# Kernel tuning notes

Measured on AMD Instinct MI355X. Metric: run time of the kernel, lower is better.

Reference implementation:

```python
import jax, jax.numpy as jnp
import numpy as np

B, S, D, H, V, C = 64, 512, 512, 512, 32000, 1000
FF = 1024

def setup_inputs() -> dict:
    key = jax.random.key(0)
    ks = jax.random.split(key, 12)
    s = 0.02
    return {
        "tokens": jax.random.randint(ks[0], (B, S), 0, V),
        "emb": jax.random.normal(ks[1], (V, D), jnp.float32) * s,
        "Wx": jax.random.normal(ks[2], (D, H), jnp.float32) * s,
        "Wh": jax.random.normal(ks[3], (H, H), jnp.float32) * s,
        "b_rnn": jnp.zeros((H,), jnp.float32),
        "W1": jax.random.normal(ks[4], (H, FF), jnp.float32) * s,
        "b1": jnp.zeros((FF,), jnp.float32),
        "W2": jax.random.normal(ks[5], (FF, FF), jnp.float32) * s,
        "b2": jnp.zeros((FF,), jnp.float32),
        "Wo": jax.random.normal(ks[6], (FF, C), jnp.float32) * s,
        "bo": jnp.zeros((C,), jnp.float32),
    }

def reference(tokens, emb, Wx, Wh, b_rnn, W1, b1, W2, b2, Wo, bo):
    # Embedding with mask_zero=True: token 0 is a masked timestep
    x = emb[tokens]                                   # [B,S,D]
    mask = (tokens != 0)                              # [B,S]
    # Precompute input projection for all timesteps (hoisted out of the scan)
    xproj = jnp.einsum('bsd,dh->bsh', x, Wx) + b_rnn  # [B,S,H]

    def step(h, inp):
        xp, m = inp                                   # [B,H], [B]
        h_new = jax.nn.relu(xp + h @ Wh)
        # Keras masking: masked steps carry previous state forward
        h = jnp.where(m[:, None], h_new, h)
        return h, None

    h0 = jnp.zeros((B, H), xproj.dtype)
    h, _ = jax.lax.scan(step, h0, (xproj.transpose(1, 0, 2), mask.T))

    y = jax.nn.relu(h @ W1 + b1)
    y = jax.nn.relu(y @ W2 + b2)
    return jax.nn.softmax(y @ Wo + bo, axis=-1)       # [B,C]
```

## Files before the change

kernel.cpp:

```cpp
#include <hip/hip_runtime.h>
#include <stdint.h>

typedef _Float16 half2_t __attribute__((ext_vector_type(2)));
typedef short bf16x8 __attribute__((ext_vector_type(8)));
typedef float f32x4 __attribute__((ext_vector_type(4)));
typedef int i32x4 __attribute__((ext_vector_type(4)));
typedef int i32x8 __attribute__((ext_vector_type(8)));
typedef unsigned short u16;
typedef unsigned int u32;
typedef unsigned long long u64;

#define B_ 64
#define S_ 512
#define D_ 512
#define H_ 512
#define FF_ 1024
#define C_ 1000

#define SW4 128.0f
#define SH4 256.0f

__device__ __forceinline__ u16 f2bf(float f){
  u32 u = __builtin_bit_cast(u32, f);
  u = (u + 0x7FFFu + ((u >> 16) & 1u)) >> 16;
  return (u16)u;
}
__device__ __forceinline__ u32 pkbf(float a, float b){
  return (u32)f2bf(a) | ((u32)f2bf(b) << 16);
}
__device__ __forceinline__ u32 packh2(float a, float b){
  u16 lo = __builtin_bit_cast(u16, (_Float16)a);
  u16 hi = __builtin_bit_cast(u16, (_Float16)b);
  return (u32)lo | ((u32)hi << 16);
}
__device__ __forceinline__ float fdot2u(u32 a, u32 b, float c){
  return __builtin_amdgcn_fdot2(__builtin_bit_cast(half2_t, a),
                                __builtin_bit_cast(half2_t, b), c, false);
}
__device__ __forceinline__ float h2f(u16 h){
  return (float)__builtin_bit_cast(_Float16, h);
}
__device__ __forceinline__ float fp4val(u32 c){
  int e = (c >> 1) & 3;
  float m = 1.0f + 0.5f * (float)(c & 1);
  return (e == 0) ? 0.5f * (float)(c & 1) : m * (float)(1 << (e - 1));
}

__global__ void k_trans_cvt(const float* __restrict__ src, u16* __restrict__ dst){
  __shared__ u16 t[64][65];
  int bx = blockIdx.x & 7, by = blockIdx.x >> 3;
  int tid = threadIdx.x;
  int c = tid & 63, r0 = (tid >> 6) * 16;
  #pragma unroll
  for (int i = 0; i < 16; i++){
    int k = by * 64 + r0 + i, n = bx * 64 + c;
    t[r0 + i][c] = f2bf(src[k * 512 + n]);
  }
  __syncthreads();
  #pragma unroll
  for (int i = 0; i < 16; i++){
    int n = bx * 64 + r0 + i, k = by * 64 + c;
    dst[n * 512 + k] = t[c][r0 + i];
  }
}

__global__ void k_prep_w4(const float* __restrict__ Wh, uint4* __restrict__ Wf4){
  int g = blockIdx.x * 256 + threadIdx.x;
  int fidx = g >> 6, l = g & 63;
  int wv = fidx >> 4, ct = (fidx >> 2) & 3, kt = fidx & 3;
  int q = l >> 4, n = wv * 64 + ct * 16 + (l & 15);
  int k0 = kt * 128 + q * 32;
  u32 d[4] = {0u, 0u, 0u, 0u};
  #pragma unroll
  for (int j = 0; j < 32; j++){
    float w = Wh[(size_t)(k0 + j) * 512 + n] * SW4;
    float aw = fabsf(w);
    u32 s = (w < 0.f) ? 8u : 0u;
    u32 c;
    if (aw < 2.f) c = (u32)(int)rintf(aw * 2.f);
    else if (aw < 4.f) c = 4u + (u32)(int)rintf(aw - 2.f);
    else { c = 6u + (u32)(int)rintf((aw - 4.f) * 0.5f); if (c > 7u) c = 7u; }
    d[j >> 3] |= (c | s) << (4 * (j & 7));
  }
  uint4 o; o.x = d[0]; o.y = d[1]; o.z = d[2]; o.w = d[3];
  Wf4[(size_t)fidx * 64 + l] = o;
}

__global__ void k_mask(const int* __restrict__ tokens, unsigned char* __restrict__ masks8){
  int i = blockIdx.x * 256 + threadIdx.x;
  masks8[i] = (tokens[i] != 0) ? 1 : 0;
}

__global__ void k_pack_pairs(const float* __restrict__ src, u32* __restrict__ dst, int N){
  int n = blockIdx.x * 256 + threadIdx.x;
  int p = blockIdx.y;
  if (n >= N) return;
  dst[p * N + n] = packh2(src[(2 * p) * N + n], src[(2 * p + 1) * N + n]);
}

__global__ __launch_bounds__(256) void k_gemm(const int* __restrict__ tokens,
                                              const float* __restrict__ emb,
                                              const u16* __restrict__ Bt,
                                              const float* __restrict__ bias,
                                              u16* __restrict__ out){
  __shared__ __align__(16) u16 As[128 * 40];
  __shared__ __align__(16) u16 Bs[128 * 40];
  int tid = threadIdx.x;
  int m0 = blockIdx.x * 128, n0 = blockIdx.y * 128;
  int w = tid >> 6, l = tid & 63;
  int wr = w >> 1, wc = w & 1;
  int kg = l >> 4, r16 = l & 15;
  f32x4 acc[4][4];
  #pragma unroll
  for (int mi = 0; mi < 4; mi++)
    #pragma unroll
    for (int ni = 0; ni < 4; ni++) acc[mi][ni] = (f32x4){0.f, 0.f, 0.f, 0.f};
  int srow = tid >> 1, spart = tid & 1;
  int tk = tokens[m0 + srow];
  for (int kt = 0; kt < 512; kt += 32){
    const float4* se = (const float4*)(emb + (size_t)tk * 512 + kt + spart * 16);
    float4 f0 = se[0], f1 = se[1], f2 = se[2], f3 = se[3];
    uint4 a0, a1;
    a0.x = pkbf(f0.x, f0.y); a0.y = pkbf(f0.z, f0.w);
    a0.z = pkbf(f1.x, f1.y); a0.w = pkbf(f1.z, f1.w);
    a1.x = pkbf(f2.x, f2.y); a1.y = pkbf(f2.z, f2.w);
    a1.z = pkbf(f3.x, f3.y); a1.w = pkbf(f3.z, f3.w);
    const uint4* sb = (const uint4*)(Bt + (size_t)(n0 + srow) * 512 + kt);
    uint4 b0 = sb[spart * 2], b1 = sb[spart * 2 + 1];
    uint4* da = (uint4*)(As + srow * 40 + spart * 16);
    da[0] = a0; da[1] = a1;
    uint4* db = (uint4*)(Bs + srow * 40 + spart * 16);
    db[0] = b0; db[1] = b1;
    __syncthreads();
    bf16x8 af[4], bfr[4];
    #pragma unroll
    for (int mi = 0; mi < 4; mi++)
      af[mi] = *(const bf16x8*)(As + (wr * 64 + mi * 16 + r16) * 40 + kg * 8);
    #pragma unroll
    for (int ni = 0; ni < 4; ni++)
      bfr[ni] = *(const bf16x8*)(Bs + (wc * 64 + ni * 16 + r16) * 40 + kg * 8);
    #pragma unroll
    for (int mi = 0; mi < 4; mi++)
      #pragma unroll
      for (int ni = 0; ni < 4; ni++)
        acc[mi][ni] = __builtin_amdgcn_mfma_f32_16x16x32_bf16(af[mi], bfr[ni], acc[mi][ni], 0, 0, 0);
    __syncthreads();
  }
  #pragma unroll
  for (int ni = 0; ni < 4; ni++){
    int col = n0 + wc * 64 + ni * 16 + r16;
    float bb = bias[col];
    #pragma unroll
    for (int mi = 0; mi < 4; mi++){
      int mb = m0 + wr * 64 + mi * 16 + kg * 4;
      #pragma unroll
      for (int r = 0; r < 4; r++){
        float v = (acc[mi][ni][r] + bb) * SH4;
        out[(size_t)(mb + r) * 512 + col] = __builtin_bit_cast(u16, (_Float16)v);
      }
    }
  }
}

__global__ __launch_bounds__(512, 2) void k_rnn(
    const uint4* __restrict__ Wf4, const u16* __restrict__ xproj,
    const unsigned char* __restrict__ masks8, u32* __restrict__ hpack){
  __shared__ __align__(16) unsigned char g4[2][256];
  __shared__ unsigned char msk[512];
  int b = blockIdx.x, tid = threadIdx.x;
  int wv = tid >> 6, l = tid & 63, q = l >> 4, n16 = l & 15;
  int col = wv * 64 + q * 16 + n16;

  i32x8 wgt[16];
  #pragma unroll
  for (int ct = 0; ct < 4; ct++)
    #pragma unroll
    for (int kt = 0; kt < 4; kt++){
      int fidx = (wv * 4 + ct) * 4 + kt;
      uint4 wl = Wf4[(size_t)fidx * 64 + l];
      i32x8 w8 = {(int)wl.x, (int)wl.y, (int)wl.z, (int)wl.w, 0, 0, 0, 0};
      wgt[ct * 4 + kt] = w8;
    }

  msk[tid] = masks8[b * 512 + tid];
  if (tid < 64) ((u32*)g4[0])[tid] = 0;
  __syncthreads();

  const u16* xp = xproj + (size_t)b * S_ * H_;
  u16 xraw = xp[col];
  u32 greg = 0;

  #pragma unroll 1
  for (int t = 0; t < 512; t++){
    u16 xnext = 0;
    if (t < 511) xnext = xp[(size_t)(t + 1) * 512 + col];
    bool wr = msk[t] != 0;
    const unsigned char* gc = g4[t & 1];

    f32x4 acc0 = {0.f,0.f,0.f,0.f}, acc1 = {0.f,0.f,0.f,0.f};
    f32x4 acc2 = {0.f,0.f,0.f,0.f}, acc3 = {0.f,0.f,0.f,0.f};
    #pragma unroll
    for (int kt = 0; kt < 4; kt++){
      i32x4 av = *(const i32x4*)(gc + kt * 64 + q * 16);
      i32x8 a8 = {av[0], av[1], av[2], av[3], 0, 0, 0, 0};
      acc0 = __builtin_amdgcn_mfma_scale_f32_16x16x128_f8f6f4(
          a8, wgt[0 * 4 + kt], acc0, 4, 4, 0, 127, 0, 127);
      acc1 = __builtin_amdgcn_mfma_scale_f32_16x16x128_f8f6f4(
          a8, wgt[1 * 4 + kt], acc1, 4, 4, 0, 127, 0, 127);
      acc2 = __builtin_amdgcn_mfma_scale_f32_16x16x128_f8f6f4(
          a8, wgt[2 * 4 + kt], acc2, 4, 4, 0, 127, 0, 127);
      acc3 = __builtin_amdgcn_mfma_scale_f32_16x16x128_f8f6f4(
          a8, wgt[3 * 4 + kt], acc3, 4, 4, 0, 127, 0, 127);
    }

    float av = (q == 0) ? acc0[0] : (q == 1) ? acc1[0] : (q == 2) ? acc2[0] : acc3[0];
    float gn = fmaxf(fmaf(av, 1.0f / SW4, h2f(xraw)), 0.f);
    u32 code;
    if (gn < 2.f) code = (u32)(int)rintf(gn * 2.f);
    else if (gn < 4.f) code = 4u + (u32)(int)rintf(gn - 2.f);
    else { u32 c = 6u + (u32)(int)rintf((gn - 4.f) * 0.5f); code = c > 7u ? 7u : c; }
    u32 pc = (u32)__shfl_xor((int)code, 1);
    u32 byte = (n16 & 1) ? (pc | (code << 4)) : (code | (pc << 4));
    if (wr) greg = byte;
    if ((l & 1) == 0) g4[(t + 1) & 1][col >> 1] = (unsigned char)greg;
    xraw = xnext;
    __syncthreads();
  }

  if (tid < 256){
    u32 byte = g4[0][tid];
    float f0 = fp4val(byte & 15u) * (1.0f / SH4);
    float f1 = fp4val(byte >> 4) * (1.0f / SH4);
    hpack[b * 256 + tid] = packh2(f0, f1);
  }
}

__global__ __launch_bounds__(256) void k_tail(const u32* __restrict__ hpack,
    const u32* __restrict__ W1p, const float* __restrict__ b1,
    const u32* __restrict__ W2p, const float* __restrict__ b2,
    const u32* __restrict__ Wop, const float* __restrict__ bo,
    float* __restrict__ out){
  __shared__ __align__(16) u32 rowA[512];
  __shared__ __align__(16) u32 rowB[512];
  __shared__ float redm[4], reds[4];
  int b = blockIdx.x, tid = threadIdx.x;
  rowA[tid] = hpack[b * 256 + tid];
  __syncthreads();

  float s0 = 0.f, s1 = 0.f, s2 = 0.f, s3 = 0.f;
  #pragma unroll 2
  for (int p = 0; p < 256; p += 4){
    uint4 h4 = *(const uint4*)&rowA[p];
    const u32* wp = W1p + (size_t)p * FF_ + tid;
    s0 = fdot2u(wp[0], h4.x, s0); s1 = fdot2u(wp[256], h4.x, s1);
    s2 = fdot2u(wp[512], h4.x, s2); s3 = fdot2u(wp[768], h4.x, s3);
    s0 = fdot2u(wp[FF_ + 0], h4.y, s0); s1 = fdot2u(wp[FF_ + 256], h4.y, s1);
    s2 = fdot2u(wp[FF_ + 512], h4.y, s2); s3 = fdot2u(wp[FF_ + 768], h4.y, s3);
    s0 = fdot2u(wp[2*FF_ + 0], h4.z, s0); s1 = fdot2u(wp[2*FF_ + 256], h4.z, s1);
    s2 = fdot2u(wp[2*FF_ + 512], h4.z, s2); s3 = fdot2u(wp[2*FF_ + 768], h4.z, s3);
    s0 = fdot2u(wp[3*FF_ + 0], h4.w, s0); s1 = fdot2u(wp[3*FF_ + 256], h4.w, s1);
    s2 = fdot2u(wp[3*FF_ + 512], h4.w, s2); s3 = fdot2u(wp[3*FF_ + 768], h4.w, s3);
  }
  {
    float y0 = fmaxf(s0 + b1[tid], 0.f);
    float y1 = fmaxf(s1 + b1[tid + 256], 0.f);
    float y2 = fmaxf(s2 + b1[tid + 512], 0.f);
    float y3 = fmaxf(s3 + b1[tid + 768], 0.f);
    float o0 = __shfl_xor(y0, 1), o1 = __shfl_xor(y1, 1);
    float o2 = __shfl_xor(y2, 1), o3 = __shfl_xor(y3, 1);
    if ((tid & 1) == 0){
      int i = tid >> 1;
      rowB[i] = packh2(y0, o0); rowB[128 + i] = packh2(y1, o1);
      rowB[256 + i] = packh2(y2, o2); rowB[384 + i] = packh2(y3, o3);
    }
  }
  __syncthreads();

  s0 = s1 = s2 = s3 = 0.f;
  #pragma unroll 2
  for (int p = 0; p < 512; p += 4){
    uint4 h4 = *(const uint4*)&rowB[p];
    const u32* wp = W2p + (size_t)p * FF_ + tid;
    s0 = fdot2u(wp[0], h4.x, s0); s1 = fdot2u(wp[256], h4.x, s1);
    s2 = fdot2u(wp[512], h4.x, s2); s3 = fdot2u(wp[768], h4.x, s3);
    s0 = fdot2u(wp[FF_ + 0], h4.y, s0); s1 = fdot2u(wp[FF_ + 256], h4.y, s1);
    s2 = fdot2u(wp[FF_ + 512], h4.y, s2); s3 = fdot2u(wp[FF_ + 768], h4.y, s3);
    s0 = fdot2u(wp[2*FF_ + 0], h4.z, s0); s1 = fdot2u(wp[2*FF_ + 256], h4.z, s1);
    s2 = fdot2u(wp[2*FF_ + 512], h4.z, s2); s3 = fdot2u(wp[2*FF_ + 768], h4.z, s3);
    s0 = fdot2u(wp[3*FF_ + 0], h4.w, s0); s1 = fdot2u(wp[3*FF_ + 256], h4.w, s1);
    s2 = fdot2u(wp[3*FF_ + 512], h4.w, s2); s3 = fdot2u(wp[3*FF_ + 768], h4.w, s3);
  }
  {
    float y0 = fmaxf(s0 + b2[tid], 0.f);
    float y1 = fmaxf(s1 + b2[tid + 256], 0.f);
    float y2 = fmaxf(s2 + b2[tid + 512], 0.f);
    float y3 = fmaxf(s3 + b2[tid + 768], 0.f);
    float o0 = __shfl_xor(y0, 1), o1 = __shfl_xor(y1, 1);
    float o2 = __shfl_xor(y2, 1), o3 = __shfl_xor(y3, 1);
    if ((tid & 1) == 0){
      int i = tid >> 1;
      rowA[i] = packh2(y0, o0); rowA[128 + i] = packh2(y1, o1);
      rowA[256 + i] = packh2(y2, o2); rowA[384 + i] = packh2(y3, o3);
    }
  }
  __syncthreads();

  int n0 = tid, n1 = tid + 256, n2 = tid + 512, n3 = tid + 768;
  bool v3 = n3 < C_;
  int n3c = v3 ? n3 : 0;
  float z0 = 0.f, z1 = 0.f, z2 = 0.f, z3 = 0.f;
  #pragma unroll 4
  for (int p = 0; p < 512; p++){
    u32 y = rowA[p];
    z0 = fdot2u(Wop[p * C_ + n0], y, z0);
    z1 = fdot2u(Wop[p * C_ + n1], y, z1);
    z2 = fdot2u(Wop[p * C_ + n2], y, z2);
    z3 = fdot2u(Wop[p * C_ + n3c], y, z3);
  }
  z0 += bo[n0]; z1 += bo[n1]; z2 += bo[n2]; z3 += bo[n3c];
  float mx = fmaxf(fmaxf(z0, z1), z2);
  if (v3) mx = fmaxf(mx, z3);
  #pragma unroll
  for (int o = 1; o < 64; o <<= 1) mx = fmaxf(mx, __shfl_xor(mx, o));
  if ((tid & 63) == 0) redm[tid >> 6] = mx;
  __syncthreads();
  mx = fmaxf(fmaxf(redm[0], redm[1]), fmaxf(redm[2], redm[3]));
  float e0 = __expf(z0 - mx), e1 = __expf(z1 - mx), e2 = __expf(z2 - mx);
  float e3 = v3 ? __expf(z3 - mx) : 0.f;
  float s = e0 + e1 + e2 + e3;
  #pragma unroll
  for (int o = 1; o < 64; o <<= 1) s += __shfl_xor(s, o);
  if ((tid & 63) == 0) reds[tid >> 6] = s;
  __syncthreads();
  s = reds[0] + reds[1] + reds[2] + reds[3];
  float inv = 1.0f / s;
  out[b * C_ + n0] = e0 * inv;
  out[b * C_ + n1] = e1 * inv;
  out[b * C_ + n2] = e2 * inv;
  if (v3) out[b * C_ + n3] = e3 * inv;
}

extern "C" void kernel_launch(void* const* d_in, const int* in_sizes, int n_in,
                              void* d_out, int out_size, void* d_ws, size_t ws_size,
                              hipStream_t stream) {
  const int*   tokens = (const int*)d_in[0];
  const float* emb    = (const float*)d_in[1];
  const float* Wx     = (const float*)d_in[2];
  const float* Wh     = (const float*)d_in[3];
  const float* brnn   = (const float*)d_in[4];
  const float* W1     = (const float*)d_in[5];
  const float* b1     = (const float*)d_in[6];
  const float* W2     = (const float*)d_in[7];
  const float* b2     = (const float*)d_in[8];
  const float* Wo     = (const float*)d_in[9];
  const float* bo     = (const float*)d_in[10];
  float* out = (float*)d_out;

  char* ws = (char*)d_ws;
  size_t off = 0;
  auto alloc = [&](size_t bytes) -> void* {
    void* p = ws + off;
    off += (bytes + 255) & ~(size_t)255;
    return p;
  };
  u16* WxT    = (u16*)alloc((size_t)512 * 512 * 2);
  u16* xproj  = (u16*)alloc((size_t)32768 * 512 * 2);
  uint4* Wf4  = (uint4*)alloc((size_t)128 * 64 * 16);
  unsigned char* masks8 = (unsigned char*)alloc(32768);
  u32* W1p    = (u32*)alloc((size_t)256 * 1024 * 4);
  u32* W2p    = (u32*)alloc((size_t)512 * 1024 * 4);
  u32* Wop    = (u32*)alloc((size_t)512 * 1000 * 4);
  u32* hpack  = (u32*)alloc((size_t)64 * 256 * 4);

  k_trans_cvt<<<dim3(64), dim3(256), 0, stream>>>(Wx, WxT);
  k_prep_w4<<<dim3(32), dim3(256), 0, stream>>>(Wh, Wf4);
  k_mask<<<dim3(128), dim3(256), 0, stream>>>(tokens, masks8);
  k_pack_pairs<<<dim3(4, 256), dim3(256), 0, stream>>>(W1, W1p, 1024);
  k_pack_pairs<<<dim3(4, 512), dim3(256), 0, stream>>>(W2, W2p, 1024);
  k_pack_pairs<<<dim3(4, 512), dim3(256), 0, stream>>>(Wo, Wop, 1000);
  k_gemm<<<dim3(256, 4), dim3(256), 0, stream>>>(tokens, emb, WxT, brnn, xproj);
  k_rnn<<<dim3(64), dim3(512), 0, stream>>>(Wf4, xproj, masks8, hpack);
  k_tail<<<dim3(64), dim3(256), 0, stream>>>(hpack, W1p, b1, W2p, b2, Wop, bo, out);
}
```

Measured before the change: 421.7 us.

## Pre-convert embedding table to bf16 and load GEMM fragments directly from global

Adds a kernel that converts the whole 32000x512 embedding table to bf16 once per call. The input-projection GEMM then reads MFMA fragments straight from global memory, with no shared-memory staging or barriers, and each block covers all 512 output columns for 64 rows. The goal is to drop the per-tile fp32-to-bf16 conversion and the __syncthreads stalls. In exchange it converts the full 65MB table even though only 32768 rows are gathered, and the global fragment loads are less coalesced.

```diff
diff --git a/kernel.cpp b/kernel.cpp
--- a/kernel.cpp
+++ b/kernel.cpp
@@ -16,6 +16,7 @@
 #define H_ 512
 #define FF_ 1024
 #define C_ 1000
+#define V_ 32000
 
 #define SW4 128.0f
 #define SH4 256.0f
@@ -44,6 +45,16 @@
   int e = (c >> 1) & 3;
   float m = 1.0f + 0.5f * (float)(c & 1);
   return (e == 0) ? 0.5f * (float)(c & 1) : m * (float)(1 << (e - 1));
+}
+
+__global__ void k_cvt_emb(const float* __restrict__ src, u16* __restrict__ dst){
+  int c = blockIdx.x * 256 + threadIdx.x;
+  const float4* s = (const float4*)(src + (size_t)c * 8);
+  float4 a = s[0], b = s[1];
+  uint4 o;
+  o.x = pkbf(a.x, a.y); o.y = pkbf(a.z, a.w);
+  o.z = pkbf(b.x, b.y); o.w = pkbf(b.z, b.w);
+  *(uint4*)(dst + (size_t)c * 8) = o;
 }
 
 __global__ void k_trans_cvt(const float* __restrict__ src, u16* __restrict__ dst){
@@ -98,61 +109,51 @@
   dst[p * N + n] = packh2(src[(2 * p) * N + n], src[(2 * p + 1) * N + n]);
 }
 
-__global__ __launch_bounds__(256) void k_gemm(const int* __restrict__ tokens,
-                                              const float* __restrict__ emb,
-                                              const u16* __restrict__ Bt,
+__global__ __launch_bounds__(512) void k_gemm(const int* __restrict__ tokens,
+                                              const u16* __restrict__ embbf,
+                                              const u16* __restrict__ WxT,
                                               const float* __restrict__ bias,
                                               u16* __restrict__ out){
-  __shared__ __align__(16) u16 As[128 * 40];
-  __shared__ __align__(16) u16 Bs[128 * 40];
   int tid = threadIdx.x;
-  int m0 = blockIdx.x * 128, n0 = blockIdx.y * 128;
-  int w = tid >> 6, l = tid & 63;
-  int wr = w >> 1, wc = w & 1;
-  int kg = l >> 4, r16 = l & 15;
+  int m0 = blockIdx.x * 64;
+  int w = tid >> 6, l = tid & 63, kg = l >> 4, r16 = l & 15;
+  const u16* aptr[4];
+  const u16* bptr[4];
+  #pragma unroll
+  for (int mi = 0; mi < 4; mi++){
+    int tok = tokens[m0 + mi * 16 + r16];
+    aptr[mi] = embbf + (size_t)tok * 512 + kg * 8;
+  }
+  #pragma unroll
+  for (int ni = 0; ni < 4; ni++)
+    bptr[ni] = WxT + (size_t)(w * 64 + ni * 16 + r16) * 512 + kg * 8;
   f32x4 acc[4][4];
   #pragma unroll
   for (int mi = 0; mi < 4; mi++)
     #pragma unroll
     for (int ni = 0; ni < 4; ni++) acc[mi][ni] = (f32x4){0.f, 0.f, 0.f, 0.f};
-  int srow = tid >> 1, spart = tid & 1;
-  int tk = tokens[m0 + srow];
-  for (int kt = 0; kt < 512; kt += 32){
-    const float4* se = (const float4*)(emb + (size_t)tk * 512 + kt + spart * 16);
-    float4 f0 = se[0], f1 = se[1], f2 = se[2], f3 = se[3];
-    uint4 a0, a1;
-    a0.x = pkbf(f0.x, f0.y); a0.y = pkbf(f0.z, f0.w);
-    a0.z = pkbf(f1.x, f1.y); a0.w = pkbf(f1.z, f1.w);
-    a1.x = pkbf(f2.x, f2.y); a1.y = pkbf(f2.z, f2.w);
-    a1.z = pkbf(f3.x, f3.y); a1.w = pkbf(f3.z, f3.w);
-    const uint4* sb = (const uint4*)(Bt + (size_t)(n0 + srow) * 512 + kt);
-    uint4 b0 = sb[spart * 2], b1 = sb[spart * 2 + 1];
-    uint4* da = (uint4*)(As + srow * 40 + spart * 16);
-    da[0] = a0; da[1] = a1;
-    uint4* db = (uint4*)(Bs + srow * 40 + spart * 16);
-    db[0] = b0; db[1] = b1;
-    __syncthreads();
+  #pragma unroll 4
+  for (int kt = 0; kt < 16; kt++){
     bf16x8 af[4], bfr[4];
     #pragma unroll
     for (int mi = 0; mi < 4; mi++)
-      af[mi] = *(const bf16x8*)(As + (wr * 64 + mi * 16 + r16) * 40 + kg * 8);
+      af[mi] = *(const bf16x8*)(aptr[mi] + kt * 32);
     #pragma unroll
     for (int ni = 0; ni < 4; ni++)
-      bfr[ni] = *(const bf16x8*)(Bs + (wc * 64 + ni * 16 + r16) * 40 + kg * 8);
+      bfr[ni] = *(const bf16x8*)(bptr[ni] + kt * 32);
     #pragma unroll
     for (int mi = 0; mi < 4; mi++)
       #pragma unroll
       for (int ni = 0; ni < 4; ni++)
         acc[mi][ni] = __builtin_amdgcn_mfma_f32_16x16x32_bf16(af[mi], bfr[ni], acc[mi][ni], 0, 0, 0);
-    __syncthreads();
   }
   #pragma unroll
   for (int ni = 0; ni < 4; ni++){
-    int col = n0 + wc * 64 + ni * 16 + r16;
+    int col = w * 64 + ni * 16 + r16;
     float bb = bias[col];
     #pragma unroll
     for (int mi = 0; mi < 4; mi++){
-      int mb = m0 + wr * 64 + mi * 16 + kg * 4;
+      int mb = m0 + mi * 16 + kg * 4;
       #pragma unroll
       for (int r = 0; r < 4; r++){
         float v = (acc[mi][ni][r] + bb) * SH4;
@@ -363,6 +364,7 @@
     off += (bytes + 255) & ~(size_t)255;
     return p;
   };
+  u16* embbf  = (u16*)alloc((size_t)V_ * 512 * 2);
   u16* WxT    = (u16*)alloc((size_t)512 * 512 * 2);
   u16* xproj  = (u16*)alloc((size_t)32768 * 512 * 2);
   uint4* Wf4  = (uint4*)alloc((size_t)128 * 64 * 16);
@@ -372,13 +374,14 @@
   u32* Wop    = (u32*)alloc((size_t)512 * 1000 * 4);
   u32* hpack  = (u32*)alloc((size_t)64 * 256 * 4);
 
+  k_cvt_emb<<<dim3(8000), dim3(256), 0, stream>>>(emb, embbf);
   k_trans_cvt<<<dim3(64), dim3(256), 0, stream>>>(Wx, WxT);
   k_prep_w4<<<dim3(32), dim3(256), 0, stream>>>(Wh, Wf4);
   k_mask<<<dim3(128), dim3(256), 0, stream>>>(tokens, masks8);
   k_pack_pairs<<<dim3(4, 256), dim3(256), 0, stream>>>(W1, W1p, 1024);
   k_pack_pairs<<<dim3(4, 512), dim3(256), 0, stream>>>(W2, W2p, 1024);
   k_pack_pairs<<<dim3(4, 512), dim3(256), 0, stream>>>(Wo, Wop, 1000);
-  k_gemm<<<dim3(256, 4), dim3(256), 0, stream>>>(tokens, emb, WxT, brnn, xproj);
+  k_gemm<<<dim3(512), dim3(512), 0, stream>>>(tokens, embbf, WxT, brnn, xproj);
   k_rnn<<<dim3(64), dim3(512), 0, stream>>>(Wf4, xproj, masks8, hpack);
   k_tail<<<dim3(64), dim3(256), 0, stream>>>(hpack, W1p, b1, W2p, b2, Wop, bo, out);
 }
```

Measured after the change: 451.3 us. 1.07x slower.
